# Kernel tuning notes

Hardware: AMD Instinct MI355X
Metric: run time of the kernel (lower is better)

Reference implementation:

```python
import jax, jax.numpy as jnp
import numpy as np

N = 50000       # num_nodes
E = 800000      # num_edges (avg degree 16)
DIN = 128       # input_dim
DOUT = 128      # output_dim
H = 4           # num_heads
HD = DOUT // H  # head_dim = 32


def setup_inputs() -> dict:
    key = jax.random.key(0)
    ks = jax.random.split(key, 9)
    x = jax.random.normal(ks[0], (N, DIN), dtype=jnp.float32)
    edge_index = jax.random.randint(ks[1], (2, E), 0, N, dtype=jnp.int64)
    s = 1.0 / np.sqrt(DIN)
    Wq = jax.random.uniform(ks[2], (DOUT, DIN), jnp.float32, -s, s)
    bq = jax.random.uniform(ks[3], (DOUT,), jnp.float32, -s, s)
    Wk = jax.random.uniform(ks[4], (DOUT, DIN), jnp.float32, -s, s)
    bk = jax.random.uniform(ks[5], (DOUT,), jnp.float32, -s, s)
    Wv = jax.random.uniform(ks[6], (DOUT, DIN), jnp.float32, -s, s)
    bv = jax.random.uniform(ks[7], (DOUT,), jnp.float32, -s, s)
    att = jax.random.normal(ks[8], (H, 2 * HD), dtype=jnp.float32)  # nn.Parameter(randn)
    return {"x": x, "edge_index": edge_index, "Wq": Wq, "bq": bq,
            "Wk": Wk, "bk": bk, "Wv": Wv, "bv": bv, "att": att}


def reference(x, edge_index, Wq, bq, Wk, bk, Wv, bv, att):
    n = x.shape[0]
    q = (x @ Wq.T + bq).reshape(n, H, HD)
    k = (x @ Wk.T + bk).reshape(n, H, HD)
    v = (x @ Wv.T + bv).reshape(n, H, HD)
    row, col = edge_index[0], edge_index[1]

    # scores = leaky_relu(sum(cat([q[row],k[col]]) * att)) computed without concat
    a_q, a_k = att[:, :HD], att[:, HD:]                       # [H,HD] each
    scores = jnp.einsum('ehd,hd->eh', q[row], a_q) \
           + jnp.einsum('ehd,hd->eh', k[col], a_k)            # [E,H]
    scores = jax.nn.leaky_relu(scores, 0.2)

    # segment-softmax over edges grouped by destination node (col), per head
    m = jax.ops.segment_max(scores, col, num_segments=n)      # [N,H]
    m = jnp.where(jnp.isfinite(m), m, 0.0)                    # empty segments -> -inf guard
    e = jnp.exp(scores - m[col])                              # [E,H]
    denom = jax.ops.segment_sum(e, col, num_segments=n)       # [N,H]
    w_edge = e / denom[col]                                   # softmax per dst segment

    # attention_weights[i] = mean over incoming edges of softmax weights; 0 if deg==0
    deg = jax.ops.segment_sum(jnp.ones((col.shape[0],), jnp.float32), col,
                              num_segments=n)                 # [N]
    w_sum = jax.ops.segment_sum(w_edge, col, num_segments=n)  # [N,H]
    attn_w = jnp.where(deg[:, None] > 0, w_sum / jnp.maximum(deg, 1.0)[:, None], 0.0)

    # output[dst] += attn_w[dst] * v[src], summed over edges
    msgs = attn_w[col][:, :, None] * v[row]                   # [E,H,HD]
    out = jax.ops.segment_sum(msgs, col, num_segments=n)      # [N,H,HD]
    return out.reshape(n, DOUT)                               # dropout: eval mode (identity)
```

## Files before the change

### kernel.cpp

```cpp
#include <hip/hip_runtime.h>


#define N_NODES 50000
#define N_EDGES 800000
#define SPAN    96
#define NBUCK   521
#define CAP     2304
#define NREP    4
#define RCAP    576
#define HSPAN   48
#define EPB     2048
#define NCHUNK  391
#define GEMMB   391

#define OFF_SORTED 12800000
#define OFF_CURSOR 17601536

typedef __attribute__((ext_vector_type(8))) short short8;
typedef __attribute__((ext_vector_type(4))) float f32x4;

__device__ __forceinline__ unsigned int pack_bf16_rne(float a, float b) {
    unsigned int ua = __float_as_uint(a), ub = __float_as_uint(b);
    unsigned int ha = (ua + 0x7FFFu + ((ua >> 16) & 1u)) >> 16;
    unsigned int hb = (ub + 0x7FFFu + ((ub >> 16) & 1u)) >> 16;
    return ha | (hb << 16);
}
__device__ __forceinline__ unsigned short bf16_rne(float a) {
    unsigned int ua = __float_as_uint(a);
    return (unsigned short)((ua + 0x7FFFu + ((ua >> 16) & 1u)) >> 16);
}
__device__ __forceinline__ float bflo(unsigned int u) { return __uint_as_float(u << 16); }
__device__ __forceinline__ float bfhi(unsigned int u) { return __uint_as_float(u & 0xFFFF0000u); }

__global__ __launch_bounds__(512) void fused_gemm_scatter(
        const float* __restrict__ x, const float* __restrict__ Wv,
        const float* __restrict__ bv, unsigned int* __restrict__ vh,
        const int* __restrict__ ei, unsigned int* __restrict__ Cursor,
        unsigned int* __restrict__ sorted) {
    __shared__ __align__(16) unsigned char smem[128 * 68 * 4];
    __shared__ int s_wide;
    int t = threadIdx.x;

    if (blockIdx.x < GEMMB) {
        unsigned int* wB = (unsigned int*)smem;
        for (int q = t; q < 8192; q += 512) {
            int o = q >> 6, k2 = q & 63;
            float2 wp = ((const float2*)Wv)[q];
            wB[o * 68 + k2] = pack_bf16_rne(wp.x, wp.y);
        }
        __syncthreads();

        int lane = t & 63, w = t >> 6;
        int quad = lane >> 4, lc = lane & 15;
        int n0 = blockIdx.x * 128 + w * 16;

        int arow = n0 + lc;
        int arowc = min(arow, N_NODES - 1);
        const float4* xrow = (const float4*)(x + (size_t)arowc * 128);

        f32x4 acc[8];
        #pragma unroll
        for (int ot = 0; ot < 8; ++ot) acc[ot] = (f32x4){0.f, 0.f, 0.f, 0.f};

        #pragma unroll
        for (int ks = 0; ks < 4; ++ks) {
            float4 f0 = xrow[ks * 8 + quad * 2];
            float4 f1 = xrow[ks * 8 + quad * 2 + 1];
            uint4 a4;
            a4.x = pack_bf16_rne(f0.x, f0.y);
            a4.y = pack_bf16_rne(f0.z, f0.w);
            a4.z = pack_bf16_rne(f1.x, f1.y);
            a4.w = pack_bf16_rne(f1.z, f1.w);
            short8 af = *(const short8*)&a4;
            #pragma unroll
            for (int ot = 0; ot < 8; ++ot) {
                uint4 b4 = *(const uint4*)&wB[(ot * 16 + lc) * 68 + ks * 16 + quad * 4];
                short8 bf = *(const short8*)&b4;
                acc[ot] = __builtin_amdgcn_mfma_f32_16x16x32_bf16(af, bf, acc[ot], 0, 0, 0);
            }
        }

        #pragma unroll
        for (int ot = 0; ot < 8; ++ot) {
            int o = ot * 16 + lc;
            float bb = bv[o];
            #pragma unroll
            for (int r = 0; r < 4; ++r) {
                int node = n0 + quad * 4 + r;
                unsigned short u = bf16_rne(acc[ot][r] + bb);
                unsigned int partner = (unsigned int)__shfl_xor((int)u, 1, 64);
                if ((lane & 1) == 0 && node < N_NODES) {
                    unsigned int pair = (unsigned int)u | (partner << 16);
                    vh[(size_t)node * 64 + (o >> 1)] = pair;
                }
            }
        }
    } else {
        unsigned int* w = (unsigned int*)smem;
        int* h    = (int*)(smem + EPB * 4);
        int* base = (int*)(smem + EPB * 4 + NBUCK * 4);
        unsigned int V = Cursor[NREP * NBUCK];
        int rep = (blockIdx.x - GEMMB) & (NREP - 1);
        for (int j = t; j < NBUCK; j += 512) h[j] = 0;
        if (t < 64) {
            int nz = (ei[2 * t + 1] != 0) ? 1 : 0;
            unsigned long long b = __ballot(nz);
            if (t == 0) s_wide = (b == 0ULL) ? 1 : 0;
        }
        __syncthreads();
        int wide = s_wide;
        int e0 = (blockIdx.x - GEMMB) * EPB;

        #pragma unroll
        for (int k = 0; k < EPB / 512; ++k) {
            int e = e0 + k * 512 + t;
            if (e < N_EDGES) {
                int r, c;
                if (wide) {
                    r = (int)((const uint2*)ei)[e].x;
                    c = (int)((const uint2*)ei)[N_EDGES + e].x;
                } else {
                    r = ei[e];
                    c = ei[N_EDGES + e];
                }
                w[k * 512 + t] = ((unsigned int)c << 16) | (unsigned int)r;
                atomicAdd(&h[c / SPAN], 1);
            } else {
                w[k * 512 + t] = 0xFFFFFFFFu;
            }
        }
        __syncthreads();
        for (int j = t; j < NBUCK; j += 512) {
            int cnt = h[j];
            base[j] = cnt ? (int)(atomicAdd(&Cursor[rep * NBUCK + j],
                                            (unsigned int)cnt) - V) : 0;
            h[j] = 0;
        }
        __syncthreads();
        #pragma unroll
        for (int k = 0; k < EPB / 512; ++k) {
            unsigned int ww = w[k * 512 + t];
            if (ww != 0xFFFFFFFFu) {
                int bin = (int)(ww >> 16) / SPAN;
                int p = base[bin] + atomicAdd(&h[bin], 1);
                if (p >= 0 && p < RCAP)
                    sorted[(size_t)bin * CAP + rep * RCAP + p] = ww;
            }
        }
    }
}

__global__ __launch_bounds__(512) void gather_kernel(const unsigned int* __restrict__ vh,
                                                     const unsigned int* __restrict__ sorted,
                                                     const unsigned int* __restrict__ Cursor,
                                                     float* __restrict__ out) {
    __shared__ unsigned int ww[CAP];
    __shared__ unsigned short rl[CAP];
    __shared__ int deg[HSPAN];
    __shared__ int startc[HSPAN];
    __shared__ int curp[HSPAN];
    __shared__ int s_off[NREP + 1];
    int t = threadIdx.x;
    int b  = blockIdx.x >> 1;
    int hb = blockIdx.x & 1;
    int nb0 = b * SPAN + hb * HSPAN;
    int span = min(HSPAN, N_NODES - nb0);
    if (span <= 0) return;
    unsigned int V = Cursor[NREP * NBUCK];
    if (t == 0) {
        int off = 0;
        #pragma unroll
        for (int rp = 0; rp < NREP; ++rp) {
            s_off[rp] = off;
            off += min((int)(Cursor[rp * NBUCK + b] - V), RCAP);
        }
        s_off[NREP] = off;
    }
    if (t < HSPAN) deg[t] = 0;
    __syncthreads();

    #pragma unroll
    for (int rp = 0; rp < NREP; ++rp) {
        int o0 = s_off[rp], cr = s_off[rp + 1] - o0;
        const unsigned int* runr = sorted + (size_t)b * CAP + rp * RCAP;
        for (int i = t; i < cr; i += 512) {
            unsigned int v = runr[i];
            ww[o0 + i] = v;
            unsigned int ln = (v >> 16) - (unsigned int)nb0;
            if (ln < (unsigned int)HSPAN) atomicAdd(&deg[ln], 1);
        }
    }
    __syncthreads();
    int cnt = s_off[NREP];

    if (t < 64) {
        int v = (t < HSPAN) ? deg[t] : 0;
        int s = v;
        #pragma unroll
        for (int off = 1; off < 64; off <<= 1) {
            int y = __shfl_up(s, off, 64);
            if (t >= off) s += y;
        }
        if (t < HSPAN) { startc[t] = s - v; curp[t] = 0; }
    }
    __syncthreads();

    for (int i = t; i < cnt; i += 512) {
        unsigned int v = ww[i];
        unsigned int ln = (v >> 16) - (unsigned int)nb0;
        if (ln < (unsigned int)HSPAN) {
            int p = startc[ln] + atomicAdd(&curp[ln], 1);
            rl[p] = (unsigned short)(v & 0xFFFFu);
        }
    }
    __syncthreads();

    int lane = t & 63, wid = t >> 6;
    int quad = lane >> 4;
    int li = lane & 15;
    const uint4* v4 = (const uint4*)vh;

#define ACC8(p) do { \
        c0 += (double)bflo((p).x); c1 += (double)bfhi((p).x); \
        c2 += (double)bflo((p).y); c3 += (double)bfhi((p).y); \
        c4 += (double)bflo((p).z); c5 += (double)bfhi((p).z); \
        c6 += (double)bflo((p).w); c7 += (double)bfhi((p).w); } while (0)

    for (int g = wid; g * 4 < span; g += 8) {
        int ln = g * 4 + quad;
        int s0 = startc[ln], d = deg[ln];
        double c0 = 0., c1 = 0., c2 = 0., c3 = 0.;
        double c4 = 0., c5 = 0., c6 = 0., c7 = 0.;
        int j = 0;
        if (d >= 8) {
            int a0 = rl[s0 + 0], a1 = rl[s0 + 1];
            int a2 = rl[s0 + 2], a3 = rl[s0 + 3];
            uint4 pA0 = v4[(size_t)a0 * 16 + li];
            uint4 pA1 = v4[(size_t)a1 * 16 + li];
            uint4 pA2 = v4[(size_t)a2 * 16 + li];
            uint4 pA3 = v4[(size_t)a3 * 16 + li];
            for (; j + 8 <= d; j += 4) {
                int b0 = rl[s0 + j + 4], b1 = rl[s0 + j + 5];
                int b2 = rl[s0 + j + 6], b3 = rl[s0 + j + 7];
                uint4 pB0 = v4[(size_t)b0 * 16 + li];
                uint4 pB1 = v4[(size_t)b1 * 16 + li];
                uint4 pB2 = v4[(size_t)b2 * 16 + li];
                uint4 pB3 = v4[(size_t)b3 * 16 + li];
                ACC8(pA0); ACC8(pA1); ACC8(pA2); ACC8(pA3);
                pA0 = pB0; pA1 = pB1; pA2 = pB2; pA3 = pB3;
            }
            ACC8(pA0); ACC8(pA1); ACC8(pA2); ACC8(pA3);
            j += 4;
        } else if (d >= 4) {
            int a0 = rl[s0 + 0], a1 = rl[s0 + 1];
            int a2 = rl[s0 + 2], a3 = rl[s0 + 3];
            uint4 pA0 = v4[(size_t)a0 * 16 + li];
            uint4 pA1 = v4[(size_t)a1 * 16 + li];
            uint4 pA2 = v4[(size_t)a2 * 16 + li];
            uint4 pA3 = v4[(size_t)a3 * 16 + li];
            ACC8(pA0); ACC8(pA1); ACC8(pA2); ACC8(pA3);
            j = 4;
        }
        for (; j < d; ++j) {
            int r0 = rl[s0 + j];
            uint4 p0 = v4[(size_t)r0 * 16 + li];
            ACC8(p0);
        }
        double sc = (d > 0) ? 1.0 / (double)d : 0.0;
        float4 ra = {(float)(c0 * sc), (float)(c1 * sc),
                     (float)(c2 * sc), (float)(c3 * sc)};
        float4 rb = {(float)(c4 * sc), (float)(c5 * sc),
                     (float)(c6 * sc), (float)(c7 * sc)};
        ((float4*)out)[(size_t)(nb0 + ln) * 32 + 2 * li]     = ra;
        ((float4*)out)[(size_t)(nb0 + ln) * 32 + 2 * li + 1] = rb;
    }
#undef ACC8
}

extern "C" void kernel_launch(void* const* d_in, const int* in_sizes, int n_in,
                              void* d_out, int out_size, void* d_ws, size_t ws_size,
                              hipStream_t stream) {
    const float* x  = (const float*)d_in[0];
    const int*   ei = (const int*)d_in[1];
    const float* Wv = (const float*)d_in[6];
    const float* bv = (const float*)d_in[7];
    float* out = (float*)d_out;

    char* ws = (char*)d_ws;
    unsigned int* vh     = (unsigned int*)(ws);
    unsigned int* sorted = (unsigned int*)(ws + OFF_SORTED);
    unsigned int* Cursor = (unsigned int*)(ws + OFF_CURSOR);

    fused_gemm_scatter<<<GEMMB + NCHUNK, 512, 0, stream>>>(x, Wv, bv, vh,
                                                           ei, Cursor, sorted);
    gather_kernel<<<NBUCK * 2, 512, 0, stream>>>(vh, sorted, Cursor, out);
}
```

Baseline: 138.5 us.

## Sub-bucket gather edges by source range to improve cache locality

Within each destination bucket, edges are now counted and placed per (destination node, source-row range of 8192). A two-level scan replaces the single-degree prefix sum. The gather loop walks source ranges in lockstep, with each wave handling two destination nodes, so that concurrently fetched value rows fall in a narrower address window and reuse cache. In exchange, the explicit four-deep load prefetch and unrolled accumulation are removed, which may reduce memory-level parallelism. It also adds extra scan synchronisation and more shared-memory atomic bins.

```diff
diff --git a/kernel.cpp b/kernel.cpp
--- a/kernel.cpp
+++ b/kernel.cpp
@@ -9,6 +9,7 @@
 #define NREP    4
 #define RCAP    576
 #define HSPAN   48
+#define NR      8
 #define EPB     2048
 #define NCHUNK  391
 #define GEMMB   391
@@ -156,10 +157,10 @@
                                                      float* __restrict__ out) {
     __shared__ unsigned int ww[CAP];
     __shared__ unsigned short rl[CAP];
-    __shared__ int deg[HSPAN];
-    __shared__ int startc[HSPAN];
-    __shared__ int curp[HSPAN];
+    __shared__ int hist[HSPAN * NR];
+    __shared__ int st[HSPAN * NR + 1];
     __shared__ int s_off[NREP + 1];
+    __shared__ int chunk_tot[6], chunk_off[6];
     int t = threadIdx.x;
     int b  = blockIdx.x >> 1;
     int hb = blockIdx.x & 1;
@@ -176,7 +177,7 @@
         }
         s_off[NREP] = off;
     }
-    if (t < HSPAN) deg[t] = 0;
+    for (int j = t; j < HSPAN * NR; j += 512) hist[j] = 0;
     __syncthreads();
 
     #pragma unroll
@@ -187,94 +188,108 @@
             unsigned int v = runr[i];
             ww[o0 + i] = v;
             unsigned int ln = (v >> 16) - (unsigned int)nb0;
-            if (ln < (unsigned int)HSPAN) atomicAdd(&deg[ln], 1);
+            if (ln < (unsigned int)HSPAN) {
+                int rr = (int)((v & 0xFFFFu) >> 13);
+                atomicAdd(&hist[ln * NR + rr], 1);
+            }
         }
     }
     __syncthreads();
     int cnt = s_off[NREP];
 
-    if (t < 64) {
-        int v = (t < HSPAN) ? deg[t] : 0;
-        int s = v;
+    int lane = t & 63, wid = t >> 6;
+    int idx = wid * 64 + lane;
+    {
+        int val = (wid < 6) ? hist[idx] : 0;
+        int s = val;
         #pragma unroll
         for (int off = 1; off < 64; off <<= 1) {
             int y = __shfl_up(s, off, 64);
-            if (t >= off) s += y;
-        }
-        if (t < HSPAN) { startc[t] = s - v; curp[t] = 0; }
-    }
-    __syncthreads();
+            if (lane >= off) s += y;
+        }
+        if (wid < 6) {
+            st[idx] = s - val;
+            if (lane == 63) chunk_tot[wid] = s;
+        }
+        __syncthreads();
+        if (t == 0) {
+            int a = 0;
+            #pragma unroll
+            for (int i = 0; i < 6; ++i) { chunk_off[i] = a; a += chunk_tot[i]; }
+            st[HSPAN * NR] = a;
+        }
+        __syncthreads();
+        if (wid < 6) { st[idx] += chunk_off[wid]; hist[idx] = 0; }
+        __syncthreads();
+    }
 
     for (int i = t; i < cnt; i += 512) {
         unsigned int v = ww[i];
         unsigned int ln = (v >> 16) - (unsigned int)nb0;
         if (ln < (unsigned int)HSPAN) {
-            int p = startc[ln] + atomicAdd(&curp[ln], 1);
+            int k = (int)ln * NR + (int)((v & 0xFFFFu) >> 13);
+            int p = st[k] + atomicAdd(&hist[k], 1);
             rl[p] = (unsigned short)(v & 0xFFFFu);
         }
     }
     __syncthreads();
 
-    int lane = t & 63, wid = t >> 6;
     int quad = lane >> 4;
     int li = lane & 15;
     const uint4* v4 = (const uint4*)vh;
 
-#define ACC8(p) do { \
-        c0 += (double)bflo((p).x); c1 += (double)bfhi((p).x); \
-        c2 += (double)bflo((p).y); c3 += (double)bfhi((p).y); \
-        c4 += (double)bflo((p).z); c5 += (double)bfhi((p).z); \
-        c6 += (double)bflo((p).w); c7 += (double)bfhi((p).w); } while (0)
-
-    for (int g = wid; g * 4 < span; g += 8) {
-        int ln = g * 4 + quad;
-        int s0 = startc[ln], d = deg[ln];
-        double c0 = 0., c1 = 0., c2 = 0., c3 = 0.;
-        double c4 = 0., c5 = 0., c6 = 0., c7 = 0.;
-        int j = 0;
-        if (d >= 8) {
-            int a0 = rl[s0 + 0], a1 = rl[s0 + 1];
-            int a2 = rl[s0 + 2], a3 = rl[s0 + 3];
-            uint4 pA0 = v4[(size_t)a0 * 16 + li];
-            uint4 pA1 = v4[(size_t)a1 * 16 + li];
-            uint4 pA2 = v4[(size_t)a2 * 16 + li];
-            uint4 pA3 = v4[(size_t)a3 * 16 + li];
-            for (; j + 8 <= d; j += 4) {
-                int b0 = rl[s0 + j + 4], b1 = rl[s0 + j + 5];
-                int b2 = rl[s0 + j + 6], b3 = rl[s0 + j + 7];
-                uint4 pB0 = v4[(size_t)b0 * 16 + li];
-                uint4 pB1 = v4[(size_t)b1 * 16 + li];
-                uint4 pB2 = v4[(size_t)b2 * 16 + li];
-                uint4 pB3 = v4[(size_t)b3 * 16 + li];
-                ACC8(pA0); ACC8(pA1); ACC8(pA2); ACC8(pA3);
-                pA0 = pB0; pA1 = pB1; pA2 = pB2; pA3 = pB3;
-            }
-            ACC8(pA0); ACC8(pA1); ACC8(pA2); ACC8(pA3);
-            j += 4;
-        } else if (d >= 4) {
-            int a0 = rl[s0 + 0], a1 = rl[s0 + 1];
-            int a2 = rl[s0 + 2], a3 = rl[s0 + 3];
-            uint4 pA0 = v4[(size_t)a0 * 16 + li];
-            uint4 pA1 = v4[(size_t)a1 * 16 + li];
-            uint4 pA2 = v4[(size_t)a2 * 16 + li];
-            uint4 pA3 = v4[(size_t)a3 * 16 + li];
-            ACC8(pA0); ACC8(pA1); ACC8(pA2); ACC8(pA3);
-            j = 4;
-        }
-        for (; j < d; ++j) {
-            int r0 = rl[s0 + j];
-            uint4 p0 = v4[(size_t)r0 * 16 + li];
-            ACC8(p0);
-        }
+    int lnA = 4 * wid + quad;
+    int lnB = lnA + 32;
+    int hasA = lnA < span;
+    int hasB = lnB < span;
+    double a0 = 0., a1 = 0., a2 = 0., a3 = 0., a4 = 0., a5 = 0., a6 = 0., a7 = 0.;
+    double b0 = 0., b1 = 0., b2 = 0., b3 = 0., b4 = 0., b5 = 0., b6 = 0., b7 = 0.;
+
+    for (int rr = 0; rr < 7; ++rr) {
+        if (hasA) {
+            int j0 = st[lnA * NR + rr], j1 = st[lnA * NR + rr + 1];
+            for (int j = j0; j < j1; ++j) {
+                int r = rl[j];
+                uint4 p = v4[(size_t)r * 16 + li];
+                a0 += (double)bflo(p.x); a1 += (double)bfhi(p.x);
+                a2 += (double)bflo(p.y); a3 += (double)bfhi(p.y);
+                a4 += (double)bflo(p.z); a5 += (double)bfhi(p.z);
+                a6 += (double)bflo(p.w); a7 += (double)bfhi(p.w);
+            }
+        }
+        if (hasB) {
+            int j0 = st[lnB * NR + rr], j1 = st[lnB * NR + rr + 1];
+            for (int j = j0; j < j1; ++j) {
+                int r = rl[j];
+                uint4 p = v4[(size_t)r * 16 + li];
+                b0 += (double)bflo(p.x); b1 += (double)bfhi(p.x);
+                b2 += (double)bflo(p.y); b3 += (double)bfhi(p.y);
+                b4 += (double)bflo(p.z); b5 += (double)bfhi(p.z);
+                b6 += (double)bflo(p.w); b7 += (double)bfhi(p.w);
+            }
+        }
+    }
+
+    if (hasA) {
+        int d = st[lnA * NR + NR] - st[lnA * NR];
         double sc = (d > 0) ? 1.0 / (double)d : 0.0;
-        float4 ra = {(float)(c0 * sc), (float)(c1 * sc),
-                     (float)(c2 * sc), (float)(c3 * sc)};
-        float4 rb = {(float)(c4 * sc), (float)(c5 * sc),
-                     (float)(c6 * sc), (float)(c7 * sc)};
-        ((float4*)out)[(size_t)(nb0 + ln) * 32 + 2 * li]     = ra;
-        ((float4*)out)[(size_t)(nb0 + ln) * 32 + 2 * li + 1] = rb;
-    }
-#undef ACC8
+        float4 ra = {(float)(a0 * sc), (float)(a1 * sc),
+                     (float)(a2 * sc), (float)(a3 * sc)};
+        float4 rb = {(float)(a4 * sc), (float)(a5 * sc),
+                     (float)(a6 * sc), (float)(a7 * sc)};
+        ((float4*)out)[(size_t)(nb0 + lnA) * 32 + 2 * li]     = ra;
+        ((float4*)out)[(size_t)(nb0 + lnA) * 32 + 2 * li + 1] = rb;
+    }
+    if (hasB) {
+        int d = st[lnB * NR + NR] - st[lnB * NR];
+        double sc = (d > 0) ? 1.0 / (double)d : 0.0;
+        float4 ra = {(float)(b0 * sc), (float)(b1 * sc),
+                     (float)(b2 * sc), (float)(b3 * sc)};
+        float4 rb = {(float)(b4 * sc), (float)(b5 * sc),
+                     (float)(b6 * sc), (float)(b7 * sc)};
+        ((float4*)out)[(size_t)(nb0 + lnB) * 32 + 2 * li]     = ra;
+        ((float4*)out)[(size_t)(nb0 + lnB) * 32 + 2 * li + 1] = rb;
+    }
 }
 
 extern "C" void kernel_launch(void* const* d_in, const int* in_sizes, int n_in,
```

New measurement: 156.1 us. 1.13x slower.
